# Kernel tuning notes

Measured on AMD Instinct MI355X. Metric: run time of the kernel, lower is better.

The kernel has to match this reference:

```python
import jax, jax.numpy as jnp
import numpy as np

B, S, D = 4, 2048, 1024
H, ADIM = 16, 64
HID = H * ADIM  # 1024


def setup_inputs() -> dict:
    key = jax.random.key(0)
    k1, k2, k3, k4 = jax.random.split(key, 4)
    iQ = jax.random.normal(k1, (B, S, D), dtype=jnp.float32)
    mask = jax.random.randint(k2, (B, S, S), 0, 2).astype(bool)
    Wa = jax.random.normal(k3, (3 * HID, D), dtype=jnp.float32) * (1.0 / np.sqrt(D))
    Wo = jax.random.normal(k4, (HID, HID), dtype=jnp.float32) * (1.0 / np.sqrt(HID))
    return {"iQ": iQ, "mask": mask, "Wa": Wa, "Wo": Wo}


def reference(iQ, mask, Wa, Wo):
    b, s, _ = iQ.shape
    # fused QKV projection: [B,S,3*HID]
    qkv = jnp.einsum("bsd,ed->bse", iQ, Wa)
    q, k, v = jnp.split(qkv, 3, axis=-1)
    # [B,S,HID] -> [B,H,S,ADIM]
    to_heads = lambda t: t.reshape(b, s, H, ADIM).transpose(0, 2, 1, 3)
    q, k, v = to_heads(q), to_heads(k), to_heads(v)
    scores = jnp.einsum("bhqd,bhkd->bhqk", q, k) / np.sqrt(ADIM).astype(np.float32)
    scores = jnp.where(mask[:, None, :, :], jnp.float32(-1e32), scores)
    attn = jax.nn.softmax(scores, axis=-1)
    o = jnp.einsum("bhqk,bhkd->bhqd", attn, v)
    o = o.transpose(0, 2, 1, 3).reshape(b, s, HID)
    return jnp.einsum("bse,oe->bso", o, Wo)
```

## Files before the change

### kernel.cpp

```cpp
#include <hip/hip_runtime.h>
#include <hip/hip_bf16.h>

typedef __bf16 bf16;
typedef __bf16 bfrag __attribute__((ext_vector_type(8)));
typedef __bf16 bf16x2 __attribute__((ext_vector_type(2)));
typedef float f32x4 __attribute__((ext_vector_type(4)));
typedef float f32x16 __attribute__((ext_vector_type(16)));
typedef unsigned u32x2 __attribute__((ext_vector_type(2)));

constexpr int Bc = 4, Sc = 2048, Hc = 16, ADc = 64, HIDc = 1024;
constexpr size_t QKV_ELEMS = (size_t)Bc * Hc * Sc * ADc;

__device__ __forceinline__ void gload_lds16(const void* g, void* lds) {
  __builtin_amdgcn_global_load_lds(
      (const __attribute__((address_space(1))) unsigned int*)g,
      (__attribute__((address_space(3))) unsigned int*)lds, 16, 0, 0);
}

__device__ __forceinline__ bfrag ldb(const bf16* p) {
  return *(const bfrag*)p;
}

__device__ __forceinline__ unsigned pack2(float lo, float hi) {
  union { bf16x2 h; unsigned u; } c;
  c.h = bf16x2{(bf16)lo, (bf16)hi};
  return c.u;
}

__device__ __forceinline__ void plswap(unsigned& a, unsigned& b) {
  u32x2 r = __builtin_amdgcn_permlane32_swap(a, b, false, false);
  a = r.x;
  b = r.y;
}

__device__ __forceinline__ f32x16 zero16() {
  f32x16 z;
#pragma unroll
  for (int i = 0; i < 16; ++i) z[i] = 0.f;
  return z;
}

__global__ __launch_bounds__(256) void f2b3(const float* __restrict__ s0,
                                            const float* __restrict__ s1,
                                            const float* __restrict__ s2,
                                            bf16* __restrict__ d0,
                                            bf16* __restrict__ d1,
                                            bf16* __restrict__ d2) {
  const int blk = blockIdx.x;
  const float* s;
  bf16* d;
  size_t base;
  if (blk < 4096)      { s = s0; d = d0; base = (size_t)blk * 2048; }
  else if (blk < 5632) { s = s1; d = d1; base = (size_t)(blk - 4096) * 2048; }
  else                 { s = s2; d = d2; base = (size_t)(blk - 5632) * 2048; }
  const size_t i = base + (size_t)threadIdx.x * 8;
  const float4 a = *(const float4*)(s + i);
  const float4 b = *(const float4*)(s + i + 4);
  bfrag o = {(bf16)a.x, (bf16)a.y, (bf16)a.z, (bf16)a.w,
             (bf16)b.x, (bf16)b.y, (bf16)b.z, (bf16)b.w};
  *(bfrag*)(d + i) = o;
}

template <int MODE>
__global__ __launch_bounds__(256) void gemm_bt(
    const bf16* __restrict__ A,
    const bf16* __restrict__ Bm,
    bf16* __restrict__ C0,
    bf16* __restrict__ C1,
    bf16* __restrict__ C2,
    float* __restrict__ Cf,
    int Kdim, int Ndim)
{
  __shared__ __align__(16) bf16 As[128 * 32];
  __shared__ __align__(16) bf16 Bs[128 * 32];

  const int tid  = threadIdx.x;
  const int wave = tid >> 6;
  const int lane = tid & 63;
  const int n16  = lane & 15;
  const int quad = lane >> 4;
  const int wm   = wave & 1;
  const int wn   = wave >> 1;
  const int m0   = blockIdx.y * 128;
  const int n0   = blockIdx.x * 128;

  const f32x4 fzero = {0.f, 0.f, 0.f, 0.f};
  f32x4 acc[4][4];
#pragma unroll
  for (int i = 0; i < 4; ++i)
#pragma unroll
    for (int j = 0; j < 4; ++j) acc[i][j] = fzero;

  const int lcol = (lane & 3) * 8;

  for (int k0 = 0; k0 < Kdim; k0 += 32) {
#pragma unroll
    for (int c = 0; c < 2; ++c) {
      const int chunk = wave * 2 + c;
      const int row   = chunk * 16 + (lane >> 2);
      const bf16* agp;
      if (MODE == 0) {
        agp = A + (size_t)(m0 + row) * Kdim + k0 + lcol;
      } else {
        const int gs = m0 + row;
        const int h  = k0 >> 6;
        agp = A + (((size_t)(gs >> 11) * Hc + h) * Sc + (gs & 2047)) * ADc
                + (k0 & 63) + lcol;
      }
      gload_lds16(agp, (char*)As + chunk * 1024);
      gload_lds16(Bm + (size_t)(n0 + row) * Kdim + k0 + lcol,
                  (char*)Bs + chunk * 1024);
    }
    __syncthreads();

    bfrag af[4], bf[4];
#pragma unroll
    for (int i = 0; i < 4; ++i)
      af[i] = ldb(As + (wm * 64 + i * 16 + n16) * 32 + quad * 8);
#pragma unroll
    for (int j = 0; j < 4; ++j)
      bf[j] = ldb(Bs + (wn * 64 + j * 16 + n16) * 32 + quad * 8);
#pragma unroll
    for (int i = 0; i < 4; ++i)
#pragma unroll
      for (int j = 0; j < 4; ++j)
        acc[i][j] = __builtin_amdgcn_mfma_f32_16x16x32_bf16(af[i], bf[j], acc[i][j], 0, 0, 0);
    __syncthreads();
  }

#pragma unroll
  for (int i = 0; i < 4; ++i) {
    const int grow = m0 + wm * 64 + i * 16 + quad * 4;
#pragma unroll
    for (int j = 0; j < 4; ++j) {
      const int col_local = wn * 64 + j * 16 + n16;
#pragma unroll
      for (int r = 0; r < 4; ++r) {
        const int row = grow + r;
        const float v = acc[i][j][r];
        if (MODE == 1) {
          Cf[(size_t)row * Ndim + n0 + col_local] = v;
        } else {
          const int seg = n0 >> 10;
          const int hid = (n0 & 1023) + col_local;
          const int h = hid >> 6, a = hid & 63;
          const int bi = row >> 11, s = row & 2047;
          if (seg == 0)
            C0[(((size_t)bi * Hc + h) * Sc + s) * ADc + a] = (bf16)(v * 0.125f);
          else if (seg == 1)
            C1[(((size_t)bi * Hc + h) * Sc + s) * ADc + a] = (bf16)v;
          else
            C2[(((size_t)bi * Hc + h) * ADc + a) * Sc + s] = (bf16)v;
        }
      }
    }
  }
}

__global__ __launch_bounds__(256) void mask_pack(const int* __restrict__ mask,
                                                 unsigned* __restrict__ bits) {
  const int w = blockIdx.x * 256 + threadIdx.x;
  const int4* p = (const int4*)(mask + (size_t)w * 32);
  unsigned out = 0;
#pragma unroll
  for (int i = 0; i < 8; ++i) {
    int4 m = p[i];
    out |= (unsigned)(m.x != 0) << (i * 4);
    out |= (unsigned)(m.y != 0) << (i * 4 + 1);
    out |= (unsigned)(m.z != 0) << (i * 4 + 2);
    out |= (unsigned)(m.w != 0) << (i * 4 + 3);
  }
  bits[w] = out;
}

__global__ __launch_bounds__(512, 4) void attn(
    const bf16* __restrict__ Qw,
    const bf16* __restrict__ Kw,
    const bf16* __restrict__ Vtw,
    const unsigned* __restrict__ mbits,
    bf16* __restrict__ Ow)
{
  __shared__ __align__(16) bf16 Ks[2][64 * 64];
  __shared__ __align__(16) bf16 Vs[2][64 * 64];

  const int tid  = threadIdx.x;
  const int wave = tid >> 6, lane = tid & 63;
  const int l31  = lane & 31, hi = lane >> 5;
  const int sw   = lane & 7;
  const int bh   = blockIdx.x >> 3, qb = blockIdx.x & 7;
  const int b    = bh >> 4;
  const int q0w  = qb * 256 + wave * 32;

  const int drow = wave * 8 + (lane >> 3);
  const int dchk = ((lane & 7) ^ (lane >> 3)) * 8;
  const bf16* gK = Kw  + ((size_t)bh * Sc + drow) * ADc + dchk;
  const bf16* gV = Vtw + ((size_t)bh * ADc + drow) * Sc + dchk;
  const int ldsb = wave * 1024;

  const bf16* qrow = Qw + ((size_t)bh * Sc + q0w + l31) * ADc + hi * 8;
  bfrag qf[4];
#pragma unroll
  for (int ks = 0; ks < 4; ++ks) qf[ks] = ldb(qrow + ks * 16);

  f32x16 of0 = zero16();
  f32x16 of1 = zero16();
  float li = 0.f;

  const unsigned* mq = mbits + ((size_t)b * Sc + q0w + l31) * (Sc / 32);

  auto tile_compute = [&](const bf16* Kbuf, const bf16* Vbuf, unsigned mx,
                          unsigned my) {
#pragma unroll
    for (int nt = 0; nt < 2; ++nt) {
      f32x16 sf = zero16();
#pragma unroll
      for (int ks = 0; ks < 4; ++ks) {
        const bfrag kf = ldb(Kbuf + (nt * 32 + l31) * 64 + (((2 * ks + hi) ^ sw) * 8));
        sf = __builtin_amdgcn_mfma_f32_32x32x16_bf16(kf, qf[ks], sf, 0, 0, 0);
      }

      const unsigned w = (nt ? my : mx) >> (hi * 4);
      unsigned D[8];
#pragma unroll
      for (int m = 0; m < 8; ++m) {
        const int r0 = 2 * m, r1 = r0 + 1;
        float p0 = __expf(sf[r0]);
        float p1 = __expf(sf[r1]);
        if ((w >> ((r0 & 3) + 8 * (r0 >> 2))) & 1u) p0 = 0.f;
        if ((w >> ((r1 & 3) + 8 * (r1 >> 2))) & 1u) p1 = 0.f;
        li += p0 + p1;
        D[m] = pack2(p0, p1);
      }

#pragma unroll
      for (int a = 0; a < 2; ++a) {
        unsigned w0 = D[4 * a + 0], w2 = D[4 * a + 2];
        plswap(w0, w2);
        unsigned w1 = D[4 * a + 1], w3 = D[4 * a + 3];
        plswap(w1, w3);
        union { unsigned u[4]; bfrag f; } pu;
        pu.u[0] = w0; pu.u[1] = w1; pu.u[2] = w2; pu.u[3] = w3;
        const int vg = ((4 * nt + 2 * a + hi) ^ sw) * 8;
        const bfrag vf0 = ldb(Vbuf + l31 * 64 + vg);
        of0 = __builtin_amdgcn_mfma_f32_32x32x16_bf16(pu.f, vf0, of0, 0, 0, 0);
        const bfrag vf1 = ldb(Vbuf + (32 + l31) * 64 + vg);
        of1 = __builtin_amdgcn_mfma_f32_32x32x16_bf16(pu.f, vf1, of1, 0, 0, 0);
      }
    }
  };

  auto stage = [&](int buf, int kt) {
    gload_lds16(gK + (size_t)kt * 64 * ADc, (char*)Ks[buf] + ldsb);
    gload_lds16(gV + (size_t)kt * 64,       (char*)Vs[buf] + ldsb);
  };

  stage(0, 0);
  __syncthreads();

  for (int kt = 0; kt < Sc / 64; ++kt) {
    const int cur = kt & 1;
    if (kt + 1 < Sc / 64) stage(cur ^ 1, kt + 1);

    const uint2 mwv = *(const uint2*)(mq + kt * 2);
    tile_compute(Ks[cur], Vs[cur], mwv.x, mwv.y);

    __syncthreads();
  }

  const float s = li + __shfl_xor(li, 32);
  const float inv = 1.f / s;
#pragma unroll
  for (int r = 0; r < 16; ++r) {
    const int query = (r & 3) + 8 * (r >> 2) + 4 * hi;
    const float invr = __shfl(inv, query);
    bf16* orow = Ow + ((size_t)bh * Sc + q0w + query) * ADc + l31;
    orow[0]  = (bf16)(of0[r] * invr);
    orow[32] = (bf16)(of1[r] * invr);
  }
}

extern "C" void kernel_launch(void* const* d_in, const int* in_sizes, int n_in,
                              void* d_out, int out_size, void* d_ws, size_t ws_size,
                              hipStream_t stream) {
  const float* iQ = (const float*)d_in[0];
  const int* mask = (const int*)d_in[1];
  const float* Wa = (const float*)d_in[2];
  const float* Wo = (const float*)d_in[3];
  float* out      = (float*)d_out;

  bf16* iQb       = (bf16*)d_out;
  bf16* Wab       = iQb + QKV_ELEMS;
  unsigned* mbits = (unsigned*)(Wab + 3145728);
  bf16* Qw  = (bf16*)d_ws;
  bf16* Kw  = Qw + QKV_ELEMS;
  bf16* Vtw = Kw + QKV_ELEMS;
  bf16* Wob = Vtw + QKV_ELEMS;

  f2b3<<<dim3(6144), 256, 0, stream>>>(iQ, Wa, Wo, iQb, Wab, Wob);
  mask_pack<<<dim3((Bc * Sc * Sc / 32) / 256), 256, 0, stream>>>(mask, mbits);
  gemm_bt<0><<<dim3(24, 64), 256, 0, stream>>>(iQb, Wab, Qw, Kw, Vtw, nullptr, 1024, 3072);
  attn<<<dim3(Bc * Hc * 8), 512, 0, stream>>>(Qw, Kw, Vtw, mbits, Qw);
  gemm_bt<1><<<dim3(8, 64), 256, 0, stream>>>(Qw, Wob, nullptr, nullptr, nullptr, out, 1024, 1024);
}
```

Before: 380.1 us.

## Fuse prep kernels, fold log2e into Q scale, MFMA row sums, reorder attn blocks

Merges the fp32-to-bf16 conversion and mask bit-packing into one launch, removing a kernel launch. Folds log2(e) into the Q scaling so the softmax can call exp2f in place of __expf. Computes softmax denominators with an extra MFMA against a ones vector, replacing per-lane scalar adds and shuffles. Remaps the attention block index so consecutive blocks cover different heads, which changes L2 locality. The extra MFMA adds matrix work per tile, and the remap may hurt or help cache reuse.

```diff
diff --git a/kernel.cpp b/kernel.cpp
--- a/kernel.cpp
+++ b/kernel.cpp
@@ -40,25 +40,42 @@
   return z;
 }
 
-__global__ __launch_bounds__(256) void f2b3(const float* __restrict__ s0,
+__global__ __launch_bounds__(256) void prep(const float* __restrict__ s0,
                                             const float* __restrict__ s1,
                                             const float* __restrict__ s2,
                                             bf16* __restrict__ d0,
                                             bf16* __restrict__ d1,
-                                            bf16* __restrict__ d2) {
+                                            bf16* __restrict__ d2,
+                                            const int* __restrict__ mask,
+                                            unsigned* __restrict__ bits) {
   const int blk = blockIdx.x;
-  const float* s;
-  bf16* d;
-  size_t base;
-  if (blk < 4096)      { s = s0; d = d0; base = (size_t)blk * 2048; }
-  else if (blk < 5632) { s = s1; d = d1; base = (size_t)(blk - 4096) * 2048; }
-  else                 { s = s2; d = d2; base = (size_t)(blk - 5632) * 2048; }
-  const size_t i = base + (size_t)threadIdx.x * 8;
-  const float4 a = *(const float4*)(s + i);
-  const float4 b = *(const float4*)(s + i + 4);
-  bfrag o = {(bf16)a.x, (bf16)a.y, (bf16)a.z, (bf16)a.w,
-             (bf16)b.x, (bf16)b.y, (bf16)b.z, (bf16)b.w};
-  *(bfrag*)(d + i) = o;
+  if (blk < 6144) {
+    const float* s;
+    bf16* d;
+    size_t base;
+    if (blk < 4096)      { s = s0; d = d0; base = (size_t)blk * 2048; }
+    else if (blk < 5632) { s = s1; d = d1; base = (size_t)(blk - 4096) * 2048; }
+    else                 { s = s2; d = d2; base = (size_t)(blk - 5632) * 2048; }
+    const size_t i = base + (size_t)threadIdx.x * 8;
+    const float4 a = *(const float4*)(s + i);
+    const float4 b = *(const float4*)(s + i + 4);
+    bfrag o = {(bf16)a.x, (bf16)a.y, (bf16)a.z, (bf16)a.w,
+               (bf16)b.x, (bf16)b.y, (bf16)b.z, (bf16)b.w};
+    *(bfrag*)(d + i) = o;
+  } else {
+    const int w = (blk - 6144) * 256 + threadIdx.x;
+    const int4* p = (const int4*)(mask + (size_t)w * 32);
+    unsigned out = 0;
+#pragma unroll
+    for (int i = 0; i < 8; ++i) {
+      int4 m = p[i];
+      out |= (unsigned)(m.x != 0) << (i * 4);
+      out |= (unsigned)(m.y != 0) << (i * 4 + 1);
+      out |= (unsigned)(m.z != 0) << (i * 4 + 2);
+      out |= (unsigned)(m.w != 0) << (i * 4 + 3);
+    }
+    bits[w] = out;
+  }
 }
 
 template <int MODE>
@@ -146,7 +163,7 @@
           const int h = hid >> 6, a = hid & 63;
           const int bi = row >> 11, s = row & 2047;
           if (seg == 0)
-            C0[(((size_t)bi * Hc + h) * Sc + s) * ADc + a] = (bf16)(v * 0.125f);
+            C0[(((size_t)bi * Hc + h) * Sc + s) * ADc + a] = (bf16)(v * 0.18033688011112042f);
           else if (seg == 1)
             C1[(((size_t)bi * Hc + h) * Sc + s) * ADc + a] = (bf16)v;
           else
@@ -155,22 +172,6 @@
       }
     }
   }
-}
-
-__global__ __launch_bounds__(256) void mask_pack(const int* __restrict__ mask,
-                                                 unsigned* __restrict__ bits) {
-  const int w = blockIdx.x * 256 + threadIdx.x;
-  const int4* p = (const int4*)(mask + (size_t)w * 32);
-  unsigned out = 0;
-#pragma unroll
-  for (int i = 0; i < 8; ++i) {
-    int4 m = p[i];
-    out |= (unsigned)(m.x != 0) << (i * 4);
-    out |= (unsigned)(m.y != 0) << (i * 4 + 1);
-    out |= (unsigned)(m.z != 0) << (i * 4 + 2);
-    out |= (unsigned)(m.w != 0) << (i * 4 + 3);
-  }
-  bits[w] = out;
 }
 
 __global__ __launch_bounds__(512, 4) void attn(
@@ -187,7 +188,7 @@
   const int wave = tid >> 6, lane = tid & 63;
   const int l31  = lane & 31, hi = lane >> 5;
   const int sw   = lane & 7;
-  const int bh   = blockIdx.x >> 3, qb = blockIdx.x & 7;
+  const int bh   = blockIdx.x & 63, qb = blockIdx.x >> 6;
   const int b    = bh >> 4;
   const int q0w  = qb * 256 + wave * 32;
 
@@ -202,9 +203,13 @@
 #pragma unroll
   for (int ks = 0; ks < 4; ++ks) qf[ks] = ldb(qrow + ks * 16);
 
-  f32x16 of0 = zero16();
-  f32x16 of1 = zero16();
-  float li = 0.f;
+  bfrag onef;
+#pragma unroll
+  for (int i = 0; i < 8; ++i) onef[i] = (bf16)1.0f;
+
+  f32x16 of0  = zero16();
+  f32x16 of1  = zero16();
+  f32x16 dacc = zero16();
 
   const unsigned* mq = mbits + ((size_t)b * Sc + q0w + l31) * (Sc / 32);
 
@@ -224,11 +229,10 @@
 #pragma unroll
       for (int m = 0; m < 8; ++m) {
         const int r0 = 2 * m, r1 = r0 + 1;
-        float p0 = __expf(sf[r0]);
-        float p1 = __expf(sf[r1]);
+        float p0 = exp2f(sf[r0]);
+        float p1 = exp2f(sf[r1]);
         if ((w >> ((r0 & 3) + 8 * (r0 >> 2))) & 1u) p0 = 0.f;
         if ((w >> ((r1 & 3) + 8 * (r1 >> 2))) & 1u) p1 = 0.f;
-        li += p0 + p1;
         D[m] = pack2(p0, p1);
       }
 
@@ -245,6 +249,7 @@
         of0 = __builtin_amdgcn_mfma_f32_32x32x16_bf16(pu.f, vf0, of0, 0, 0, 0);
         const bfrag vf1 = ldb(Vbuf + (32 + l31) * 64 + vg);
         of1 = __builtin_amdgcn_mfma_f32_32x32x16_bf16(pu.f, vf1, of1, 0, 0, 0);
+        dacc = __builtin_amdgcn_mfma_f32_32x32x16_bf16(pu.f, onef, dacc, 0, 0, 0);
       }
     }
   };
@@ -267,12 +272,10 @@
     __syncthreads();
   }
 
-  const float s = li + __shfl_xor(li, 32);
-  const float inv = 1.f / s;
 #pragma unroll
   for (int r = 0; r < 16; ++r) {
     const int query = (r & 3) + 8 * (r >> 2) + 4 * hi;
-    const float invr = __shfl(inv, query);
+    const float invr = 1.f / dacc[r];
     bf16* orow = Ow + ((size_t)bh * Sc + q0w + query) * ADc + l31;
     orow[0]  = (bf16)(of0[r] * invr);
     orow[32] = (bf16)(of1[r] * invr);
@@ -296,8 +299,7 @@
   bf16* Vtw = Kw + QKV_ELEMS;
   bf16* Wob = Vtw + QKV_ELEMS;
 
-  f2b3<<<dim3(6144), 256, 0, stream>>>(iQ, Wa, Wo, iQb, Wab, Wob);
-  mask_pack<<<dim3((Bc * Sc * Sc / 32) / 256), 256, 0, stream>>>(mask, mbits);
+  prep<<<dim3(8192), 256, 0, stream>>>(iQ, Wa, Wo, iQb, Wab, Wob, mask, mbits);
   gemm_bt<0><<<dim3(24, 64), 256, 0, stream>>>(iQb, Wab, Qw, Kw, Vtw, nullptr, 1024, 3072);
   attn<<<dim3(Bc * Hc * 8), 512, 0, stream>>>(Qw, Kw, Vtw, mbits, Qw);
   gemm_bt<1><<<dim3(8, 64), 256, 0, stream>>>(Qw, Wob, nullptr, nullptr, nullptr, out, 1024, 1024);
```

Measured after the change: 402.2 us. +5.8%, slower.
